# Kernel tuning notes

Hardware: AMD Instinct MI355X
Metric: run time of the kernel (lower is better)

Reference implementation:

```python
import jax, jax.numpy as jnp
import numpy as np

B, OBS, ACT, NT, E, H1, H2, D = 4096, 390, 20, 10, 8, 1024, 512, 256


def setup_inputs() -> dict:
    key = jax.random.key(0)
    ks = jax.random.split(key, 16)
    f32 = jnp.float32

    def w(k, shape, fan_in):
        return jax.random.normal(k, shape, f32) / np.float32(np.sqrt(fan_in))

    return {
        "state_feat": jax.random.normal(ks[0], (B, OBS), f32),
        "act": jax.random.normal(ks[1], (B, ACT), f32),
        "task_id": jax.random.randint(ks[2], (B,), 0, NT, jnp.int32),
        "rep_W1": w(ks[3], (OBS + ACT, H1), OBS + ACT),
        "rep_b1": jnp.zeros((H1,), f32),
        "rep_W2": w(ks[4], (H1, H1), H1),
        "rep_b2": jnp.zeros((H1,), f32),
        "emb": 0.5 * jax.random.normal(ks[5], (NT, D), f32),
        "kW1": w(ks[6], (E, H1, H2), H1),
        "kb1": jnp.zeros((E, H2), f32),
        "kW2": w(ks[7], (E, H2, D), H2),
        "kb2": jnp.zeros((E, D), f32),
        "vW1": w(ks[8], (E, H1, H2), H1),
        "vb1": jnp.zeros((E, H2), f32),
        "vW2": w(ks[9], (E, H2, D), H2),
        "vb2": jnp.zeros((E, D), f32),
        "tW1": w(ks[10], (D, D), D),
        "tb1": jnp.zeros((D,), f32),
        "tW2": w(ks[11], (D, D), D),
        "tb2": jnp.zeros((D,), f32),
        "tW3": w(ks[12], (D, 1), D),
        "tb3": jnp.zeros((1,), f32),
    }


def reference(state_feat, act, task_id, rep_W1, rep_b1, rep_W2, rep_b2, emb,
              kW1, kb1, kW2, kb2, vW1, vb1, vW2, vb2,
              tW1, tb1, tW2, tb2, tW3, tb3):
    # representation: mlp([obs+act, 1024, 1024]) -> ReLU on first layer only
    x = jnp.concatenate([state_feat, act], axis=-1)              # [B, 410]
    rep = jnp.maximum(x @ rep_W1 + rep_b1, 0.0) @ rep_W2 + rep_b2  # [B, H1]
    query = jnp.tanh(emb[task_id])                               # [B, D]

    # batched per-expert key/value MLPs (grouped GEMM instead of python loop)
    hk = jnp.maximum(jnp.einsum('bi,eio->ebo', rep, kW1) + kb1[:, None, :], 0.0)
    keys = jnp.einsum('ebo,eod->ebd', hk, kW2) + kb2[:, None, :]   # [E, B, D]
    hv = jnp.maximum(jnp.einsum('bi,eio->ebo', rep, vW1) + vb1[:, None, :], 0.0)
    vals = jnp.einsum('ebo,eod->ebd', hv, vW2) + vb2[:, None, :]   # [E, B, D]

    scores = jnp.einsum('bd,ebd->be', query, keys)               # [B, E]
    weight = jax.nn.softmax(scores, axis=1)                      # [B, E]
    tower_in = jnp.einsum('be,ebd->bd', weight, vals)            # [B, D]

    # tower: mlp([256, 256, 256, 1]) -> ReLU, ReLU, Identity
    h = jnp.maximum(tower_in @ tW1 + tb1, 0.0)
    h = jnp.maximum(h @ tW2 + tb2, 0.0)
    q = (h @ tW3 + tb3)[:, 0]                                    # [B]

    expert_loss = -jnp.mean(
        jnp.sum(jnp.clip(jnp.log(weight + 1e-10), -6.0, 0.0), axis=-1) * 0.3)
    return q, expert_loss
```

## Files before the change

### kernel.cpp

```cpp
#include <hip/hip_runtime.h>

constexpr int Bn   = 4096;
constexpr int OBS  = 390;
constexpr int ACTN = 20;
constexpr int IN   = 410;
constexpr int KPAD = 416;
constexpr int E    = 8;
constexpr int NT   = 10;
constexpr int H1   = 1024;
constexpr int H2   = 512;
constexpr int D    = 256;

typedef __bf16 bf16x8 __attribute__((ext_vector_type(8)));
typedef float  f32x4  __attribute__((ext_vector_type(4)));
typedef unsigned short u16x8 __attribute__((ext_vector_type(8)));

__device__ __forceinline__ unsigned short f2bf(float f) {
    unsigned int u = __float_as_uint(f);
    unsigned int r = u + 0x7fffu + ((u >> 16) & 1u);
    return (unsigned short)(r >> 16);
}
__device__ __forceinline__ float bf2f(unsigned short h) {
    return __uint_as_float(((unsigned int)h) << 16);
}
__device__ __forceinline__ void gload16(void* lds_dst, const void* g_src) {
    __builtin_amdgcn_global_load_lds(
        (const __attribute__((address_space(1))) void*)g_src,
        (__attribute__((address_space(3))) void*)lds_dst,
        16, 0, 0);
}

struct TD2 {
    const float* W;
    unsigned short* WT;
    int K, Kpad, N;
    long long gsW, gsO;
    int tilesN, perG, start;
};
struct TD2Arr { TD2 d[8]; };

__global__ __launch_bounds__(256) void tc64(TD2Arr da) {
    int bid = blockIdx.x;
    int i = 0;
#pragma unroll
    for (int j = 1; j < 8; ++j) if (bid >= da.d[j].start) i = j;
    TD2 dd = da.d[i];
    int local = bid - dd.start;
    int g   = local / dd.perG;
    int rem = local - g * dd.perG;
    int kt  = rem / dd.tilesN;
    int nt  = rem - kt * dd.tilesN;
    const float* W = dd.W + (long long)g * dd.gsW;
    unsigned short* WT = dd.WT + (long long)g * dd.gsO;
    int k0 = kt * 64, n0 = nt * 64;

    __shared__ float tile[64][68];
    int t = threadIdx.x;
    {
        int kl  = t >> 4;
        int nl4 = (t & 15) * 4;
#pragma unroll
        for (int r = 0; r < 4; ++r) {
            int k = k0 + kl + r * 16;
            float4 v = make_float4(0.f, 0.f, 0.f, 0.f);
            if (k < dd.K) v = *(const float4*)(W + (long long)k * dd.N + n0 + nl4);
            *(float4*)&tile[kl + r * 16][nl4] = v;
        }
    }
    __syncthreads();
    int nl = t >> 2, kc = (t & 3) * 16;
    if (k0 + kc < dd.Kpad) {
        u16x8 o0, o1;
#pragma unroll
        for (int j = 0; j < 8; ++j) {
            o0[j] = f2bf(tile[kc + j][nl]);
            o1[j] = f2bf(tile[kc + 8 + j][nl]);
        }
        unsigned short* dst = WT + (long long)(n0 + nl) * dd.Kpad + k0 + kc;
        *(u16x8*)dst       = o0;
        *(u16x8*)(dst + 8) = o1;
    }
}

constexpr int PREPB = (Bn * KPAD) / 256;

__global__ __launch_bounds__(256) void misc_kernel(
    const float* __restrict__ sf, const float* __restrict__ ac,
    unsigned short* __restrict__ x,
    const float* __restrict__ kW2, const float* __restrict__ kb2,
    const float* __restrict__ emb, float* __restrict__ qp, float* __restrict__ qb,
    const float* __restrict__ kb1, const float* __restrict__ vb1,
    float* __restrict__ b1cat)
{
    int bid = blockIdx.x;
    if (bid < PREPB) {
        int idx = bid * 256 + threadIdx.x;
        int b = idx / KPAD;
        int k = idx - b * KPAD;
        float v = 0.f;
        if (k < OBS) v = sf[b * OBS + k];
        else if (k < IN) v = ac[b * ACTN + (k - OBS)];
        x[idx] = f2bf(v);
        return;
    }
    if (bid < PREPB + 17) {
        int qbid = bid - PREPB;
        __shared__ float tq[NT][D];
        for (int i = threadIdx.x; i < NT * D; i += 256)
            tq[i / D][i - (i / D) * D] = tanhf(emb[i]);
        __syncthreads();
        if (qbid < 16) {
            int e = qbid >> 1;
            int h = (qbid & 1) * 256 + threadIdx.x;
            const float4* row = (const float4*)(kW2 + ((long long)e * H2 + h) * D);
            float acc[NT] = {};
            for (int d4 = 0; d4 < D / 4; ++d4) {
                float4 wv = row[d4];
#pragma unroll
                for (int t = 0; t < NT; ++t)
                    acc[t] += wv.x * tq[t][d4 * 4] + wv.y * tq[t][d4 * 4 + 1]
                            + wv.z * tq[t][d4 * 4 + 2] + wv.w * tq[t][d4 * 4 + 3];
            }
#pragma unroll
            for (int t = 0; t < NT; ++t)
                qp[((long long)e * NT + t) * H2 + h] = acc[t];
        } else if (threadIdx.x < E * NT) {
            int e = threadIdx.x / NT, t = threadIdx.x - e * NT;
            float s = 0.f;
            for (int d = 0; d < D; ++d) s += kb2[e * D + d] * tq[t][d];
            qb[e * NT + t] = s;
        }
        return;
    }
    int i = (bid - PREPB - 17) * 256 + threadIdx.x;
    b1cat[i] = (i < E * H2) ? kb1[i] : vb1[i - E * H2];
}

template <int ACTF, int OUTF, int BK>
__global__ __launch_bounds__(256) void gemm_bf16(
    const unsigned short* __restrict__ A, const unsigned short* __restrict__ BT,
    const float* __restrict__ bias, void* __restrict__ Cout,
    int K, int ldc,
    long long gsA, long long gsBT, long long gsBias, long long gsC)
{
    constexpr int CH   = BK / 8;
    constexpr int RPR  = 256 / CH;
    constexpr int RNDS = 128 / RPR;
    constexpr int TB   = 128 * BK * 2;
    constexpr int RS   = CH * 16;

    const int g = blockIdx.z;
    A    += (long long)g * gsA;
    BT   += (long long)g * gsBT;
    bias += (long long)g * gsBias;
    float*          Cf = (float*)Cout + (long long)g * gsC;
    unsigned short* Cb = (unsigned short*)Cout + (long long)g * gsC;

    __shared__ alignas(16) char smem[2 * TB];
    const int t  = threadIdx.x;
    const int w  = t >> 6, l = t & 63;
    const int lr = l & 15, lk = l >> 4;
    const int gm = blockIdx.y * 128, gn = blockIdx.x * 128;
    const int wm = (w >> 1) * 64,   wn = (w & 1) * 64;

    const int srow = t / CH;
    const int swzS = (CH == 8) ? (srow & 7) : ((srow >> 1) & 3);
    const int sc   = (t % CH) ^ swzS;
    const unsigned short* gA = A  + (long long)(gm + srow) * K + sc * 8;
    const unsigned short* gB = BT + (long long)(gn + srow) * K + sc * 8;

    const int swzL = (CH == 8) ? (lr & 7) : ((lr >> 1) & 3);
    const int aoff = (wm + lr) * RS + ((lk ^ swzL) * 16);
    const int boff = TB + (wn + lr) * RS + ((lk ^ swzL) * 16);

    f32x4 acc[4][4] = {};

    for (int k0 = 0; k0 < K; k0 += BK) {
#pragma unroll
        for (int j = 0; j < RNDS; ++j) {
            gload16(smem + j * 4096 + w * 1024,      gA + k0 + (long long)j * RPR * K);
            gload16(smem + TB + j * 4096 + w * 1024, gB + k0 + (long long)j * RPR * K);
        }
        __syncthreads();

        bf16x8 af[4], bfr[4];
#pragma unroll
        for (int i = 0; i < 4; ++i) {
            af[i]  = *(const bf16x8*)(smem + aoff + i * 16 * RS);
            bfr[i] = *(const bf16x8*)(smem + boff + i * 16 * RS);
        }
#pragma unroll
        for (int mi = 0; mi < 4; ++mi)
#pragma unroll
            for (int ni = 0; ni < 4; ++ni)
                acc[mi][ni] = __builtin_amdgcn_mfma_f32_16x16x32_bf16(
                    af[mi], bfr[ni], acc[mi][ni], 0, 0, 0);

        if constexpr (BK == 64) {
#pragma unroll
            for (int i = 0; i < 4; ++i) {
                af[i]  = *(const bf16x8*)(smem + (aoff ^ 64) + i * 16 * RS);
                bfr[i] = *(const bf16x8*)(smem + (boff ^ 64) + i * 16 * RS);
            }
#pragma unroll
            for (int mi = 0; mi < 4; ++mi)
#pragma unroll
                for (int ni = 0; ni < 4; ++ni)
                    acc[mi][ni] = __builtin_amdgcn_mfma_f32_16x16x32_bf16(
                        af[mi], bfr[ni], acc[mi][ni], 0, 0, 0);
        }
        __syncthreads();
    }

    const int orow0 = gm + wm + lk * 4;
    const int ocol0 = gn + wn + lr;
    float bv[4];
#pragma unroll
    for (int ni = 0; ni < 4; ++ni) bv[ni] = bias[gn + wn + lr + ni * 16];
#pragma unroll
    for (int mi = 0; mi < 4; ++mi)
#pragma unroll
        for (int ni = 0; ni < 4; ++ni)
#pragma unroll
            for (int r = 0; r < 4; ++r) {
                float v = acc[mi][ni][r] + bv[ni];
                if (ACTF == 1) v = fmaxf(v, 0.f);
                long long off = (long long)(orow0 + mi * 16 + r) * ldc + ocol0 + ni * 16;
                if (OUTF == 0) Cf[off] = v;
                else           Cb[off] = f2bf(v);
            }
}

template <int KTOT, int ACTF, int OUTF, int SC>
__global__ __launch_bounds__(512, 2) void gemm256(
    const unsigned short* __restrict__ A, const unsigned short* __restrict__ BT,
    const float* __restrict__ bias, void* __restrict__ Cout,
    int ldc, long long gsA, long long gsBT, long long gsBias, long long gsC,
    const int* __restrict__ task_id, const float* __restrict__ qp,
    float* __restrict__ spart)
{
    constexpr int NT_ = KTOT / 64;
    static_assert(NT_ >= 4 && (NT_ % 2) == 0, "KTOT must be multiple of 128");

    const int g = blockIdx.z;
    A    += (long long)g * gsA;
    BT   += (long long)g * gsBT;
    bias += (long long)g * gsBias;
    float*          Cf = (float*)Cout + (long long)g * gsC;
    unsigned short* Cb = (unsigned short*)Cout + (long long)g * gsC;

    __shared__ __align__(16) char smem[131072];

    const int tid = threadIdx.x;
    const int l  = tid & 63;
    const int lr = l & 15, lk = l >> 4;
    const int w  = tid >> 6;
    const int wr = w >> 2, wc = w & 3;
    const int gm = blockIdx.y * 256, gn = blockIdx.x * 256;

    const int srow = tid >> 3;
    const int cg   = (tid & 7) ^ (srow & 7);
    const unsigned short* gA = A  + (long long)(gm + srow) * KTOT + cg * 8;
    const unsigned short* gB = BT + (long long)(gn + srow) * KTOT + cg * 8;
    const int wbase = (tid & ~63) * 16;

    const int cs0 = ((0 | lk) ^ (lr & 7)) * 16;
    const int cs1 = ((4 | lk) ^ (lr & 7)) * 16;
    const int aRow = wr * 16384 + lr * 128;
    const int bRow = 32768 + (wc >> 1) * 16384 + ((wc & 1) * 64 + lr) * 128;

    f32x4 acc[8][4] = {};

    auto stA = [&](int c, int s, int kt) {
        const unsigned short* src = gA + (long long)(s * 128) * KTOT + kt * 64;
        char* d = smem + c * 65536 + s * 16384 + wbase;
        gload16(d,        src);
        gload16(d + 8192, src + (long long)64 * KTOT);
    };
    auto stB = [&](int c, int s, int kt) {
        const unsigned short* src = gB + (long long)(s * 128) * KTOT + kt * 64;
        char* d = smem + c * 65536 + 32768 + s * 16384 + wbase;
        gload16(d,        src);
        gload16(d + 8192, src + (long long)64 * KTOT);
    };

    stA(0, 0, 0); stA(0, 1, 0); stB(0, 0, 0); stB(0, 1, 0);
    stA(1, 0, 1); stA(1, 1, 1);
    asm volatile("s_waitcnt vmcnt(4)" ::: "memory");
    __builtin_amdgcn_s_barrier();
    __builtin_amdgcn_sched_barrier(0);

#pragma unroll
    for (int kt = 0; kt < NT_; ++kt) {
        const int c = kt & 1;
        const char* bufc = smem + c * 65536;
        bf16x8 a0[4], a1[4], b0[4], b1[4];

#pragma unroll
        for (int m = 0; m < 4; ++m) {
            const char* base = bufc + aRow + m * (16 * 128);
            a0[m] = *(const bf16x8*)(base + cs0);
            a1[m] = *(const bf16x8*)(base + cs1);
        }
#pragma unroll
        for (int n = 0; n < 4; ++n) {
            const char* base = bufc + bRow + n * (16 * 128);
            b0[n] = *(const bf16x8*)(base + cs0);
            b1[n] = *(const bf16x8*)(base + cs1);
        }
        if (kt + 1 < NT_) { stB(c ^ 1, 0, kt + 1); stB(c ^ 1, 1, kt + 1); }
        __builtin_amdgcn_s_setprio(1);
#pragma unroll
        for (int m = 0; m < 4; ++m)
#pragma unroll
            for (int n = 0; n < 4; ++n) {
                acc[m][n] = __builtin_amdgcn_mfma_f32_16x16x32_bf16(a0[m], b0[n], acc[m][n], 0, 0, 0);
                acc[m][n] = __builtin_amdgcn_mfma_f32_16x16x32_bf16(a1[m], b1[n], acc[m][n], 0, 0, 0);
            }
        __builtin_amdgcn_s_setprio(0);

#pragma unroll
        for (int m = 0; m < 4; ++m) {
            const char* base = bufc + aRow + (64 + m * 16) * 128;
            a0[m] = *(const bf16x8*)(base + cs0);
            a1[m] = *(const bf16x8*)(base + cs1);
        }
        asm volatile("s_waitcnt lgkmcnt(0)" ::: "memory");
        __builtin_amdgcn_sched_barrier(0);
        if (kt + 2 < NT_) {
            __builtin_amdgcn_s_barrier();
            __builtin_amdgcn_sched_barrier(0);
            stA(c, 0, kt + 2); stA(c, 1, kt + 2);
        }
        __builtin_amdgcn_s_setprio(1);
#pragma unroll
        for (int m = 0; m < 4; ++m)
#pragma unroll
            for (int n = 0; n < 4; ++n) {
                acc[4 + m][n] = __builtin_amdgcn_mfma_f32_16x16x32_bf16(a0[m], b0[n], acc[4 + m][n], 0, 0, 0);
                acc[4 + m][n] = __builtin_amdgcn_mfma_f32_16x16x32_bf16(a1[m], b1[n], acc[4 + m][n], 0, 0, 0);
            }
        __builtin_amdgcn_s_setprio(0);

        if (kt + 1 < NT_) {
            if (kt + 2 < NT_) { asm volatile("s_waitcnt vmcnt(4)" ::: "memory"); }
            else              { asm volatile("s_waitcnt vmcnt(0)" ::: "memory"); }
            __builtin_amdgcn_sched_barrier(0);
            __builtin_amdgcn_s_barrier();
            __builtin_amdgcn_sched_barrier(0);
        }
    }

    const int orow0 = gm + wr * 128 + lk * 4;
    const int ocol0 = gn + wc * 64 + lr;
    float bv[4];
#pragma unroll
    for (int ni = 0; ni < 4; ++ni) bv[ni] = bias[gn + wc * 64 + lr + ni * 16];

    if (SC && g < E) {
#pragma unroll
        for (int mi = 0; mi < 8; ++mi) {
            int tr[4];
#pragma unroll
            for (int r = 0; r < 4; ++r) tr[r] = task_id[orow0 + mi * 16 + r];
#pragma unroll
            for (int r = 0; r < 4; ++r) {
                float rp = 0.f;
#pragma unroll
                for (int ni = 0; ni < 4; ++ni) {
                    float v = acc[mi][ni][r] + bv[ni];
                    v = fmaxf(v, 0.f);
                    rp += v * qp[((long long)(g * NT + tr[r])) * H2 + ocol0 + ni * 16];
                }
                rp += __shfl_xor(rp, 1);
                rp += __shfl_xor(rp, 2);
                rp += __shfl_xor(rp, 4);
                rp += __shfl_xor(rp, 8);
                if (lr == 0)
                    spart[(((long long)g * Bn + orow0 + mi * 16 + r) << 3)
                          + (wc << 1) + blockIdx.x] = rp;
            }
        }
    } else {
#pragma unroll
        for (int mi = 0; mi < 8; ++mi)
#pragma unroll
            for (int ni = 0; ni < 4; ++ni)
#pragma unroll
                for (int r = 0; r < 4; ++r) {
                    float v = acc[mi][ni][r] + bv[ni];
                    if (ACTF == 1) v = fmaxf(v, 0.f);
                    long long off = (long long)(orow0 + mi * 16 + r) * ldc + ocol0 + ni * 16;
                    if (OUTF == 0) Cf[off] = v;
                    else           Cb[off] = f2bf(v);
                }
    }
}

__global__ __launch_bounds__(256) void attn_kernel(
    const float* __restrict__ spart, const float* __restrict__ qb,
    const int* __restrict__ task_id, const unsigned short* __restrict__ vals,
    unsigned short* __restrict__ tower_in, float* __restrict__ loss_partial)
{
    int wv   = threadIdx.x >> 6;
    int lane = threadIdx.x & 63;
    int b    = blockIdx.x * 4 + wv;
    int t    = task_id[b];

    float s[E];
#pragma unroll
    for (int e = 0; e < E; ++e) {
        const float4* sp = (const float4*)(spart + (((long long)e * Bn + b) << 3));
        float4 p0 = sp[0], p1 = sp[1];
        s[e] = p0.x + p0.y + p0.z + p0.w + p1.x + p1.y + p1.z + p1.w + qb[e * NT + t];
    }

    float m = s[0];
#pragma unroll
    for (int e = 1; e < E; ++e) m = fmaxf(m, s[e]);
    float wgt[E];
    float sum = 0.f;
#pragma unroll
    for (int e = 0; e < E; ++e) { wgt[e] = expf(s[e] - m); sum += wgt[e]; }
    float inv = 1.f / sum;

    int d0 = lane * 4;
    float4 acc = make_float4(0.f, 0.f, 0.f, 0.f);
    float lb = 0.f;
#pragma unroll
    for (int e = 0; e < E; ++e) {
        float we = wgt[e] * inv;
        uint2 vv = *(const uint2*)&vals[((long long)e * Bn + b) * D + d0];
        acc.x += we * __uint_as_float(vv.x << 16);
        acc.y += we * __uint_as_float(vv.x & 0xffff0000u);
        acc.z += we * __uint_as_float(vv.y << 16);
        acc.w += we * __uint_as_float(vv.y & 0xffff0000u);
        lb += fminf(fmaxf(logf(we + 1e-10f), -6.f), 0.f);
    }
    ushort4 o;
    o.x = f2bf(acc.x); o.y = f2bf(acc.y); o.z = f2bf(acc.z); o.w = f2bf(acc.w);
    *(ushort4*)&tower_in[(long long)b * D + d0] = o;

    __shared__ float sm[4];
    if (lane == 0) sm[wv] = lb;
    __syncthreads();
    if (threadIdx.x == 0)
        loss_partial[blockIdx.x] = sm[0] + sm[1] + sm[2] + sm[3];
}

__global__ __launch_bounds__(256) void qdot_loss_kernel(
    const float* __restrict__ t2, const float* __restrict__ tW3,
    const float* __restrict__ tb3, float* __restrict__ out,
    const float* __restrict__ lossp)
{
    if (blockIdx.x == Bn / 4) {
        float s = 0.f;
        for (int i = threadIdx.x; i < Bn / 4; i += 256) s += lossp[i];
#pragma unroll
        for (int off = 32; off > 0; off >>= 1) s += __shfl_xor(s, off, 64);
        __shared__ float sm[4];
        if ((threadIdx.x & 63) == 0) sm[threadIdx.x >> 6] = s;
        __syncthreads();
        if (threadIdx.x == 0) out[Bn] = (-0.3f / Bn) * (sm[0] + sm[1] + sm[2] + sm[3]);
        return;
    }
    int wv   = threadIdx.x >> 6;
    int lane = threadIdx.x & 63;
    int b    = blockIdx.x * 4 + wv;
    int d0   = lane * 4;
    float4 h4 = *(const float4*)&t2[(long long)b * D + d0];
    float4 w4 = *(const float4*)&tW3[d0];
    float p = h4.x * w4.x + h4.y * w4.y + h4.z * w4.z + h4.w * w4.w;
#pragma unroll
    for (int off = 32; off > 0; off >>= 1) p += __shfl_xor(p, off, 64);
    if (lane == 0) out[b] = p + tb3[0];
}

extern "C" void kernel_launch(void* const* d_in, const int* in_sizes, int n_in,
                              void* d_out, int out_size, void* d_ws, size_t ws_size,
                              hipStream_t stream) {
    const float* state_feat = (const float*)d_in[0];
    const float* act        = (const float*)d_in[1];
    const int*   task_id    = (const int*)d_in[2];
    const float* rep_W1 = (const float*)d_in[3];
    const float* rep_b1 = (const float*)d_in[4];
    const float* rep_W2 = (const float*)d_in[5];
    const float* rep_b2 = (const float*)d_in[6];
    const float* emb    = (const float*)d_in[7];
    const float* kW1 = (const float*)d_in[8];
    const float* kb1 = (const float*)d_in[9];
    const float* kW2 = (const float*)d_in[10];
    const float* kb2 = (const float*)d_in[11];
    const float* vW1 = (const float*)d_in[12];
    const float* vb1 = (const float*)d_in[13];
    const float* vW2 = (const float*)d_in[14];
    const float* vb2 = (const float*)d_in[15];
    const float* tW1 = (const float*)d_in[16];
    const float* tb1 = (const float*)d_in[17];
    const float* tW2 = (const float*)d_in[18];
    const float* tb2 = (const float*)d_in[19];
    const float* tW3 = (const float*)d_in[20];
    const float* tb3 = (const float*)d_in[21];
    float* out = (float*)d_out;

    char* p = (char*)d_ws;
    auto alloc = [&](size_t bytes) {
        char* r = p;
        p += (bytes + 255) & ~(size_t)255;
        return r;
    };
    unsigned short* x      = (unsigned short*)alloc((size_t)Bn * KPAD * 2);
    unsigned short* repW1T = (unsigned short*)alloc((size_t)H1 * KPAD * 2);
    unsigned short* repW2T = (unsigned short*)alloc((size_t)H1 * H1 * 2);
    unsigned short* w1T    = (unsigned short*)alloc((size_t)2 * E * H2 * H1 * 2);
    unsigned short* w2T    = (unsigned short*)alloc((size_t)E * D * H2 * 2);
    unsigned short* tW1T   = (unsigned short*)alloc((size_t)D * D * 2);
    unsigned short* tW2T   = (unsigned short*)alloc((size_t)D * D * 2);
    float*          b1cat  = (float*)alloc((size_t)2 * E * H2 * 4);
    float*          qp     = (float*)alloc((size_t)E * NT * H2 * 4);
    float*          qb     = (float*)alloc((size_t)E * NT * 4);
    char*           h1zone = alloc((size_t)Bn * H1 * 2);
    unsigned short* rep    = (unsigned short*)alloc((size_t)Bn * H1 * 2);
    unsigned short* hkv    = (unsigned short*)alloc((size_t)2 * E * Bn * H2 * 2);
    unsigned short* vals   = (unsigned short*)alloc((size_t)E * Bn * D * 2);
    float*          spart  = (float*)alloc((size_t)E * Bn * 8 * 4);
    float*          lossp  = (float*)alloc((size_t)(Bn / 4) * 4);

    unsigned short* h1       = (unsigned short*)h1zone;
    unsigned short* tower_in = (unsigned short*)h1zone;
    unsigned short* t1       = (unsigned short*)(h1zone + (size_t)Bn * D * 2);
    float*          t2       = (float*)(h1zone + (size_t)2 * Bn * D * 2);
    unsigned short* hv = hkv + (size_t)E * Bn * H2;

    TD2Arr da;
    int startAcc = 0;
    auto setd = [&](int i, const float* W, unsigned short* WT, int K, int Kpad, int N,
                    long long gsW, long long gsO, int groups) {
        TD2& dd = da.d[i];
        dd.W = W; dd.WT = WT; dd.K = K; dd.Kpad = Kpad; dd.N = N;
        dd.gsW = gsW; dd.gsO = gsO;
        dd.tilesN = N / 64;
        dd.perG = ((Kpad + 63) / 64) * dd.tilesN;
        dd.start = startAcc;
        startAcc += dd.perG * groups;
    };
    setd(0, rep_W1, repW1T, IN, KPAD, H1, 0, 0, 1);
    setd(1, rep_W2, repW2T, H1, H1, H1, 0, 0, 1);
    setd(2, kW1, w1T,                       H1, H1, H2, (long long)H1 * H2, (long long)H2 * H1, E);
    setd(3, vW1, w1T + (size_t)E * H2 * H1, H1, H1, H2, (long long)H1 * H2, (long long)H2 * H1, E);
    setd(4, vW2, w2T,                       H2, H2, D, (long long)H2 * D, (long long)D * H2, E);
    setd(5, tW1, tW1T, D, D, D, 0, 0, 1);
    setd(6, tW2, tW2T, D, D, D, 0, 0, 1);
    da.d[7] = da.d[6];
    da.d[7].start = 0x7fffffff;
    tc64<<<startAcc, 256, 0, stream>>>(da);

    misc_kernel<<<PREPB + 17 + 32, 256, 0, stream>>>(
        state_feat, act, x, kW2, kb2, emb, qp, qb, kb1, vb1, b1cat);

    gemm_bf16<1, 1, 32><<<dim3(H1 / 128, Bn / 128, 1), 256, 0, stream>>>(
        x, repW1T, rep_b1, h1, KPAD, H1, 0, 0, 0, 0);
    gemm_bf16<0, 1, 64><<<dim3(H1 / 128, Bn / 128, 1), 256, 0, stream>>>(
        h1, repW2T, rep_b2, rep, H1, H1, 0, 0, 0, 0);

    gemm256<H1, 1, 1, 1><<<dim3(H2 / 256, Bn / 256, 2 * E), 512, 0, stream>>>(
        rep, w1T, b1cat, hkv, H2,
        0, (long long)H2 * H1, H2, (long long)Bn * H2,
        task_id, qp, spart);
    gemm_bf16<0, 1, 64><<<dim3(D / 128, Bn / 128, E), 256, 0, stream>>>(
        hv, w2T, vb2, vals, H2, D,
        (long long)Bn * H2, (long long)D * H2, D, (long long)Bn * D);

    attn_kernel<<<Bn / 4, 256, 0, stream>>>(
        spart, qb, task_id, vals, tower_in, lossp);

    gemm_bf16<1, 1, 64><<<dim3(D / 128, Bn / 128, 1), 256, 0, stream>>>(
        tower_in, tW1T, tb1, t1, D, D, 0, 0, 0, 0);
    gemm_bf16<1, 0, 64><<<dim3(D / 128, Bn / 128, 1), 256, 0, stream>>>(
        t1, tW2T, tb2, t2, D, D, 0, 0, 0, 0);

    qdot_loss_kernel<<<Bn / 4 + 1, 256, 0, stream>>>(t2, tW3, tb3, out, lossp);
}
```

Before: 181.3 us.

## Fuse tower output dot into GEMM epilogue, stage score inputs in LDS, pad K

Adds an epilogue mode to the bf16 GEMM that multiplies the final tower layer by tW3 and reduces across lanes to per-row partials. The fp32 t2 activation is no longer written, and the final kernel only sums four partials per row. The expert-score epilogue now stages qp rows and task_ids in shared memory instead of gathering them from global memory. The first representation GEMM is padded to K=448 so it can use BK=64, which adds some zero work in exchange for fewer loop iterations.

```diff
diff --git a/kernel.cpp b/kernel.cpp
--- a/kernel.cpp
+++ b/kernel.cpp
@@ -4,7 +4,7 @@
 constexpr int OBS  = 390;
 constexpr int ACTN = 20;
 constexpr int IN   = 410;
-constexpr int KPAD = 416;
+constexpr int KPAD = 448;
 constexpr int E    = 8;
 constexpr int NT   = 10;
 constexpr int H1   = 1024;
@@ -141,7 +141,8 @@
     const unsigned short* __restrict__ A, const unsigned short* __restrict__ BT,
     const float* __restrict__ bias, void* __restrict__ Cout,
     int K, int ldc,
-    long long gsA, long long gsBT, long long gsBias, long long gsC)
+    long long gsA, long long gsBT, long long gsBias, long long gsC,
+    const float* __restrict__ tW3 = nullptr, float* __restrict__ qpart = nullptr)
 {
     constexpr int CH   = BK / 8;
     constexpr int RPR  = 256 / CH;
@@ -217,18 +218,43 @@
     float bv[4];
 #pragma unroll
     for (int ni = 0; ni < 4; ++ni) bv[ni] = bias[gn + wn + lr + ni * 16];
-#pragma unroll
-    for (int mi = 0; mi < 4; ++mi)
-#pragma unroll
-        for (int ni = 0; ni < 4; ++ni)
+
+    if (OUTF == 2) {
+        float tw3v[4];
+#pragma unroll
+        for (int ni = 0; ni < 4; ++ni) tw3v[ni] = tW3[gn + wn + lr + ni * 16];
+#pragma unroll
+        for (int mi = 0; mi < 4; ++mi)
 #pragma unroll
             for (int r = 0; r < 4; ++r) {
-                float v = acc[mi][ni][r] + bv[ni];
-                if (ACTF == 1) v = fmaxf(v, 0.f);
-                long long off = (long long)(orow0 + mi * 16 + r) * ldc + ocol0 + ni * 16;
-                if (OUTF == 0) Cf[off] = v;
-                else           Cb[off] = f2bf(v);
+                float part = 0.f;
+#pragma unroll
+                for (int ni = 0; ni < 4; ++ni) {
+                    float v = acc[mi][ni][r] + bv[ni];
+                    if (ACTF == 1) v = fmaxf(v, 0.f);
+                    part += v * tw3v[ni];
+                }
+                part += __shfl_xor(part, 1);
+                part += __shfl_xor(part, 2);
+                part += __shfl_xor(part, 4);
+                part += __shfl_xor(part, 8);
+                if (lr == 0)
+                    qpart[(orow0 + mi * 16 + r) * 4 + ((wn >> 6) << 1) + blockIdx.x] = part;
             }
+    } else {
+#pragma unroll
+        for (int mi = 0; mi < 4; ++mi)
+#pragma unroll
+            for (int ni = 0; ni < 4; ++ni)
+#pragma unroll
+                for (int r = 0; r < 4; ++r) {
+                    float v = acc[mi][ni][r] + bv[ni];
+                    if (ACTF == 1) v = fmaxf(v, 0.f);
+                    long long off = (long long)(orow0 + mi * 16 + r) * ldc + ocol0 + ni * 16;
+                    if (OUTF == 0) Cf[off] = v;
+                    else           Cb[off] = f2bf(v);
+                }
+    }
 }
 
 template <int KTOT, int ACTF, int OUTF, int SC>
@@ -358,19 +384,29 @@
     for (int ni = 0; ni < 4; ++ni) bv[ni] = bias[gn + wc * 64 + lr + ni * 16];
 
     if (SC && g < E) {
+        __syncthreads();
+        float* qpl  = (float*)smem;
+        int*   tidl = (int*)(smem + NT * 256 * 4);
+        for (int i = tid; i < NT * 256; i += 512) {
+            int tt = i >> 8, cc = i & 255;
+            qpl[i] = qp[((long long)(g * NT + tt)) * H2 + gn + cc];
+        }
+        if (tid < 256) tidl[tid] = task_id[gm + tid];
+        __syncthreads();
+
+        const int rbase = wr * 128 + lk * 4;
+        const int cbase = wc * 64 + lr;
 #pragma unroll
         for (int mi = 0; mi < 8; ++mi) {
-            int tr[4];
-#pragma unroll
-            for (int r = 0; r < 4; ++r) tr[r] = task_id[orow0 + mi * 16 + r];
 #pragma unroll
             for (int r = 0; r < 4; ++r) {
+                int trow = tidl[rbase + mi * 16 + r];
                 float rp = 0.f;
 #pragma unroll
                 for (int ni = 0; ni < 4; ++ni) {
                     float v = acc[mi][ni][r] + bv[ni];
                     v = fmaxf(v, 0.f);
-                    rp += v * qp[((long long)(g * NT + tr[r])) * H2 + ocol0 + ni * 16];
+                    rp += v * qpl[trow * 256 + cbase + ni * 16];
                 }
                 rp += __shfl_xor(rp, 1);
                 rp += __shfl_xor(rp, 2);
@@ -448,12 +484,11 @@
         loss_partial[blockIdx.x] = sm[0] + sm[1] + sm[2] + sm[3];
 }
 
-__global__ __launch_bounds__(256) void qdot_loss_kernel(
-    const float* __restrict__ t2, const float* __restrict__ tW3,
-    const float* __restrict__ tb3, float* __restrict__ out,
-    const float* __restrict__ lossp)
+__global__ __launch_bounds__(256) void qfin_kernel(
+    const float* __restrict__ qpart, const float* __restrict__ tb3,
+    float* __restrict__ out, const float* __restrict__ lossp)
 {
-    if (blockIdx.x == Bn / 4) {
+    if (blockIdx.x == Bn / 256) {
         float s = 0.f;
         for (int i = threadIdx.x; i < Bn / 4; i += 256) s += lossp[i];
 #pragma unroll
@@ -464,16 +499,9 @@
         if (threadIdx.x == 0) out[Bn] = (-0.3f / Bn) * (sm[0] + sm[1] + sm[2] + sm[3]);
         return;
     }
-    int wv   = threadIdx.x >> 6;
-    int lane = threadIdx.x & 63;
-    int b    = blockIdx.x * 4 + wv;
-    int d0   = lane * 4;
-    float4 h4 = *(const float4*)&t2[(long long)b * D + d0];
-    float4 w4 = *(const float4*)&tW3[d0];
-    float p = h4.x * w4.x + h4.y * w4.y + h4.z * w4.z + h4.w * w4.w;
-#pragma unroll
-    for (int off = 32; off > 0; off >>= 1) p += __shfl_xor(p, off, 64);
-    if (lane == 0) out[b] = p + tb3[0];
+    int b = blockIdx.x * 256 + threadIdx.x;
+    float4 qpv = *(const float4*)&qpart[b * 4];
+    out[b] = qpv.x + qpv.y + qpv.z + qpv.w + tb3[0];
 }
 
 extern "C" void kernel_launch(void* const* d_in, const int* in_sizes, int n_in,
@@ -524,12 +552,12 @@
     unsigned short* hkv    = (unsigned short*)alloc((size_t)2 * E * Bn * H2 * 2);
     unsigned short* vals   = (unsigned short*)alloc((size_t)E * Bn * D * 2);
     float*          spart  = (float*)alloc((size_t)E * Bn * 8 * 4);
+    float*          qpart  = (float*)alloc((size_t)Bn * 4 * 4);
     float*          lossp  = (float*)alloc((size_t)(Bn / 4) * 4);
 
     unsigned short* h1       = (unsigned short*)h1zone;
     unsigned short* tower_in = (unsigned short*)h1zone;
     unsigned short* t1       = (unsigned short*)(h1zone + (size_t)Bn * D * 2);
-    float*          t2       = (float*)(h1zone + (size_t)2 * Bn * D * 2);
     unsigned short* hv = hkv + (size_t)E * Bn * H2;
 
     TD2Arr da;
@@ -558,7 +586,7 @@
     misc_kernel<<<PREPB + 17 + 32, 256, 0, stream>>>(
         state_feat, act, x, kW2, kb2, emb, qp, qb, kb1, vb1, b1cat);
 
-    gemm_bf16<1, 1, 32><<<dim3(H1 / 128, Bn / 128, 1), 256, 0, stream>>>(
+    gemm_bf16<1, 1, 64><<<dim3(H1 / 128, Bn / 128, 1), 256, 0, stream>>>(
         x, repW1T, rep_b1, h1, KPAD, H1, 0, 0, 0, 0);
     gemm_bf16<0, 1, 64><<<dim3(H1 / 128, Bn / 128, 1), 256, 0, stream>>>(
         h1, repW2T, rep_b2, rep, H1, H1, 0, 0, 0, 0);
@@ -576,8 +604,8 @@
 
     gemm_bf16<1, 1, 64><<<dim3(D / 128, Bn / 128, 1), 256, 0, stream>>>(
         tower_in, tW1T, tb1, t1, D, D, 0, 0, 0, 0);
-    gemm_bf16<1, 0, 64><<<dim3(D / 128, Bn / 128, 1), 256, 0, stream>>>(
-        t1, tW2T, tb2, t2, D, D, 0, 0, 0, 0);
-
-    qdot_loss_kernel<<<Bn / 4 + 1, 256, 0, stream>>>(t2, tW3, tb3, out, lossp);
-}
+    gemm_bf16<1, 2, 64><<<dim3(D / 128, Bn / 128, 1), 256, 0, stream>>>(
+        t1, tW2T, tb2, nullptr, D, D, 0, 0, 0, 0, tW3, qpart);
+
+    qfin_kernel<<<Bn / 256 + 1, 256, 0, stream>>>(qpart, tb3, out, lossp);
+}
```

Measured after the change: 179.3 us. Within noise of the previous version (-1.1%).
